# Performance work log

Measured on AMD Instinct MI355X. Metric: run time of the kernel, lower is better.

The kernel has to match this reference:

```python
import jax, jax.numpy as jnp
import numpy as np
from jax import lax

IMG_H, IMG_W = 800, 800
FM_H, FM_W = 50, 50
SIZES = (32.0, 64.0, 128.0)
RATIOS = (0.5, 1.0, 2.0)
A = len(SIZES) * len(RATIOS)          # 9 anchors per location
PRE_NMS = 512
POST_NMS = 128
MIN_SCORE = 0.5
IOU_THRESH = 0.7
MIN_SIZE = 0.001


def gen_anchor_boxes():
    """Anchors in (x1,y1,x2,y2), location-major / anchor-minor ordering
    (matches the permute(0,2,1).reshape(-1,4) layout of the offsets)."""
    sy, sx = IMG_H / FM_H, IMG_W / FM_W
    cy = (np.arange(FM_H) + 0.5) * sy
    cx = (np.arange(FM_W) + 0.5) * sx
    whs = []
    for s in SIZES:
        for r in RATIOS:
            h = s * np.sqrt(r)
            w = s / np.sqrt(r)
            whs.append((w, h))
    whs = np.asarray(whs, np.float32)                      # [A,2]
    cyg, cxg = np.meshgrid(cy, cx, indexing='ij')          # [H,W]
    ctr = np.stack([cxg, cyg], -1)[:, :, None, :]          # [H,W,1,2] (cx,cy)
    half = whs[None, None] / 2.0                           # [1,1,A,2]
    boxes = np.concatenate([ctr - half, ctr + half], -1)   # [H,W,A,4]
    return jnp.asarray(boxes.reshape(-1, 4), jnp.float32)  # [H*W*A,4]


def conv2d(x, w, b, pad):
    y = lax.conv_general_dilated(x, w, (1, 1), [(pad, pad), (pad, pad)],
                                 dimension_numbers=('NCHW', 'OIHW', 'NCHW'))
    return y + b[None, :, None, None]


def decode_boxes(offsets, anchors):
    """offsets [B,N,4] = (dx,dy,dw,dh); anchors [N,4] corners -> corners."""
    aw = anchors[:, 2] - anchors[:, 0]
    ah = anchors[:, 3] - anchors[:, 1]
    acx = anchors[:, 0] + 0.5 * aw
    acy = anchors[:, 1] + 0.5 * ah
    px = acx + offsets[..., 0] * aw
    py = acy + offsets[..., 1] * ah
    pw = aw * jnp.exp(offsets[..., 2])
    ph = ah * jnp.exp(offsets[..., 3])
    return jnp.stack([px - 0.5 * pw, py - 0.5 * ph,
                      px + 0.5 * pw, py + 0.5 * ph], -1)


def proposals_one_image(boxes, scores):
    """boxes [N,4], scores [N] -> padded ([POST_NMS,4],[POST_NMS])."""
    s, idx = lax.top_k(scores, PRE_NMS)          # pre-NMS top-k (sorted desc)
    b = boxes[idx]                               # [PRE,4]
    b = jnp.stack([jnp.clip(b[:, 0], 0.0, IMG_W),
                   jnp.clip(b[:, 1], 0.0, IMG_H),
                   jnp.clip(b[:, 2], 0.0, IMG_W),
                   jnp.clip(b[:, 3], 0.0, IMG_H)], -1)
    w = b[:, 2] - b[:, 0]
    h = b[:, 3] - b[:, 1]
    valid = (w >= MIN_SIZE) & (h >= MIN_SIZE) & (s >= MIN_SCORE)
    # pairwise IoU (NMS decisions are discrete -> stop_gradient)
    bi = lax.stop_gradient(b)
    area = (bi[:, 2] - bi[:, 0]) * (bi[:, 3] - bi[:, 1])
    lt = jnp.maximum(bi[:, None, :2], bi[None, :, :2])
    rb = jnp.minimum(bi[:, None, 2:], bi[None, :, 2:])
    wh = jnp.clip(rb - lt, 0.0)
    inter = wh[..., 0] * wh[..., 1]
    iou = inter / (area[:, None] + area[None, :] - inter + 1e-9)
    rng = jnp.arange(PRE_NMS)

    def body(keep, i):
        sup = (iou[i] > IOU_THRESH) & (rng > i) & keep[i]
        return keep & ~sup, None

    keep, _ = lax.scan(body, valid, rng)         # greedy NMS over sorted cands
    masked = jnp.where(keep, s, -1.0)
    top_s, top_i = lax.top_k(masked, POST_NMS)   # kept boxes keep score order
    ok = top_s >= MIN_SCORE
    out_b = b[top_i] * ok[:, None].astype(b.dtype)
    out_s = jnp.where(ok, top_s, 0.0)
    return out_b, out_s


def rpn_forward(feature_maps, w1, b1, w2, b2, w3, b3):
    B = feature_maps.shape[0]
    shared = jax.nn.relu(conv2d(feature_maps, w1, b1, 1))      # [B,512,H,W]
    cls = jax.nn.sigmoid(conv2d(shared, w2, b2, 0))            # [B,A,H,W]
    off = conv2d(shared, w3, b3, 0)                            # [B,4A,H,W]
    # location-major, anchor-minor flattening (matches torch permute/reshape)
    scores = cls.reshape(B, A, -1).transpose(0, 2, 1).reshape(B, -1)        # [B,N]
    offsets = off.reshape(B, 4 * A, -1).transpose(0, 2, 1).reshape(B, -1, 4)
    anchors = gen_anchor_boxes()
    boxes = decode_boxes(offsets, anchors)                     # [B,N,4]
    return jax.vmap(proposals_one_image)(boxes, scores)        # padded outputs


def setup_inputs() -> dict:
    key = jax.random.key(0)
    ks = jax.random.split(key, 4)
    fm = jax.random.normal(ks[0], (16, 512, FM_H, FM_W), jnp.float32)
    w1 = jax.random.normal(ks[1], (512, 512, 3, 3), jnp.float32) * 0.02
    b1 = jnp.zeros((512,), jnp.float32)
    w2 = jax.random.normal(ks[2], (9, 512, 1, 1), jnp.float32) * 0.05
    b2 = jnp.zeros((9,), jnp.float32)
    w3 = jax.random.normal(ks[3], (36, 512, 1, 1), jnp.float32) * 0.01
    b3 = jnp.zeros((36,), jnp.float32)
    return {"feature_maps": fm, "w1": w1, "b1": b1, "w2": w2, "b2": b2,
            "w3": w3, "b3": b3}


def reference(feature_maps, w1, b1, w2, b2, w3, b3):
    return rpn_forward(feature_maps, w1, b1, w2, b2, w3, b3)
```

## Files before the change

### kernel.cpp

```cpp
#include <hip/hip_runtime.h>
#include <math.h>
#include <stdint.h>

#define FMW 50
#define P_IMG 2500
#define CIN 512
#define NANCH 22500
#define BATCH 16
#define PRE 512
#define POST 128
#define NCHUNK 44
#define NPAD (NCHUNK * 512)
#define MB 192
#define NTIL 14
#define WIN 320

typedef __attribute__((ext_vector_type(8))) short short8;
typedef __attribute__((ext_vector_type(16))) float f32x16;

union U4S8 { uint4 u; short8 s; };

__device__ __forceinline__ unsigned short f2bf(float x) {
    unsigned u = __float_as_uint(x);
    unsigned r = u + 0x7FFFu + ((u >> 16) & 1u);
    return (unsigned short)(r >> 16);
}
__device__ __forceinline__ float bf2f(unsigned short h) {
    return __uint_as_float(((unsigned)h) << 16);
}

__device__ __forceinline__ void gload_lds16(const void* g, void* l) {
    __builtin_amdgcn_global_load_lds(
        (const __attribute__((address_space(1))) void*)g,
        (__attribute__((address_space(3))) void*)l, 16, 0, 0);
}

__global__ void k_prepack(const float* __restrict__ w1, char* __restrict__ w1pack) {
    int t = blockIdx.x * 256 + threadIdx.x;
    int l = t & 63;
    int NT = (t >> 6) & 15;
    int c = (t >> 10) & 31;
    int pos = t >> 15;
    int oc = NT * 32 + (l & 31);
    unsigned short hv[8], lv[8];
#pragma unroll
    for (int j = 0; j < 8; ++j) {
        int ci = c * 16 + (l >> 5) * 8 + j;
        float x = w1[((size_t)oc * 512 + ci) * 9 + pos];
        unsigned short h = f2bf(x);
        hv[j] = h;
        lv[j] = f2bf(x - bf2f(h));
    }
    size_t base = ((size_t)((pos * 32 + c) * 16 + NT) * 2) * 1024 + (size_t)l * 16;
    uint4 hu, lu;
    hu.x = hv[0] | ((unsigned)hv[1] << 16); hu.y = hv[2] | ((unsigned)hv[3] << 16);
    hu.z = hv[4] | ((unsigned)hv[5] << 16); hu.w = hv[6] | ((unsigned)hv[7] << 16);
    lu.x = lv[0] | ((unsigned)lv[1] << 16); lu.y = lv[2] | ((unsigned)lv[3] << 16);
    lu.z = lv[4] | ((unsigned)lv[5] << 16); lu.w = lv[6] | ((unsigned)lv[7] << 16);
    *(uint4*)(w1pack + base) = hu;
    *(uint4*)(w1pack + base + 1024) = lu;
}

__global__ __launch_bounds__(512, 2)
void k_conv_mfma(const float* __restrict__ fm, const char* __restrict__ w1pack,
                 const float* __restrict__ b1, const float* __restrict__ w2,
                 const float* __restrict__ b2, const float* __restrict__ w3,
                 const float* __restrict__ b3,
                 float* __restrict__ off_ws, unsigned long long* __restrict__ keys) {
    __shared__ __align__(16) char smem[123392];

    const int t = threadIdx.x;
    const int l = t & 63;
    const int w = t >> 6;
    const int r = w >> 2;
    const int q = w & 3;
    const int img = blockIdx.x / NTIL;
    const int p0 = (blockIdx.x % NTIL) * MB;

    f32x16 acc[3][4];
#pragma unroll
    for (int mt = 0; mt < 3; ++mt)
#pragma unroll
        for (int nt = 0; nt < 4; ++nt)
#pragma unroll
            for (int g = 0; g < 16; ++g) acc[mt][nt][g] = 0.f;

    int xs[3];
#pragma unroll
    for (int mt = 0; mt < 3; ++mt) xs[mt] = (p0 + r * 96 + mt * 32 + (l & 31)) % FMW;

    const int arb = (64 + r * 96 + (l & 31)) * 32 + (l >> 5) * 16;
    const size_t img_base = (size_t)img * CIN * P_IMG;
    const int DPOS[9] = {-51, -50, -49, -1, 0, 1, 49, 50, 51};

    char* Abuf = smem;
    char* Bb0 = smem + 20480;
    char* Bb1 = smem + 53248;

    auto stageA = [&](int cc) {
#pragma unroll
        for (int i = 0; i < 3; ++i) {
            int flat = i * 512 + t;
            if (flat < 1280) {
                int qq = flat & 3;
                int pxl = flat >> 2;
                int pw = p0 - 64 + pxl;
                bool ok = (pw >= 0) && (pw < P_IMG);
                float v[4];
#pragma unroll
                for (int k = 0; k < 4; ++k)
                    v[k] = ok ? fm[img_base + (size_t)(cc * 16 + qq * 4 + k) * P_IMG + pw] : 0.f;
                unsigned short h[4], lo[4];
#pragma unroll
                for (int k = 0; k < 4; ++k) {
                    h[k] = f2bf(v[k]);
                    lo[k] = f2bf(v[k] - bf2f(h[k]));
                }
                uint2 hu, lu;
                hu.x = h[0] | ((unsigned)h[1] << 16);  hu.y = h[2] | ((unsigned)h[3] << 16);
                lu.x = lo[0] | ((unsigned)lo[1] << 16); lu.y = lo[2] | ((unsigned)lo[3] << 16);
                *(uint2*)(Abuf + pxl * 32 + qq * 8) = hu;
                *(uint2*)(Abuf + 10240 + pxl * 32 + qq * 8) = lu;
            }
        }
    };

    auto stageB = [&](int kk) {
        int c = kk / 9, pos = kk % 9;
        const char* src = w1pack + (size_t)(pos * 32 + c) * 32768;
        char* dst = (kk & 1) ? Bb1 : Bb0;
#pragma unroll
        for (int j = 0; j < 4; ++j) {
            int chunk = w * 4 + j;
            gload_lds16(src + chunk * 1024 + l * 16, dst + chunk * 1024);
        }
    };

    stageB(0);
    stageA(0);
    __syncthreads();

    for (int kk = 0; kk < 288; ++kk) {
        const int c = kk / 9, pos = kk % 9;
        if (kk + 1 < 288) stageB(kk + 1);

        const int dpos = DPOS[pos];
        const int dx = pos % 3 - 1;
        U4S8 ah[3], al[3];
        const char* ap = Abuf + arb + dpos * 32;
#pragma unroll
        for (int mt = 0; mt < 3; ++mt) {
            ah[mt].u = *(const uint4*)(ap + mt * 1024);
            al[mt].u = *(const uint4*)(ap + 10240 + mt * 1024);
            bool xok = (dx == 0) || (dx < 0 ? (xs[mt] > 0) : (xs[mt] < FMW - 1));
            if (!xok) {
                ah[mt].u.x = 0; ah[mt].u.y = 0; ah[mt].u.z = 0; ah[mt].u.w = 0;
                al[mt].u.x = 0; al[mt].u.y = 0; al[mt].u.z = 0; al[mt].u.w = 0;
            }
        }
        const char* bp = ((kk & 1) ? Bb1 : Bb0) + q * 8192 + l * 16;
#pragma unroll
        for (int nt = 0; nt < 4; ++nt) {
            U4S8 bh, bl;
            bh.u = *(const uint4*)(bp + nt * 2048);
            bl.u = *(const uint4*)(bp + nt * 2048 + 1024);
#pragma unroll
            for (int mt = 0; mt < 3; ++mt) {
                acc[mt][nt] = __builtin_amdgcn_mfma_f32_32x32x16_bf16(ah[mt].s, bh.s, acc[mt][nt], 0, 0, 0);
                acc[mt][nt] = __builtin_amdgcn_mfma_f32_32x32x16_bf16(al[mt].s, bh.s, acc[mt][nt], 0, 0, 0);
                acc[mt][nt] = __builtin_amdgcn_mfma_f32_32x32x16_bf16(ah[mt].s, bl.s, acc[mt][nt], 0, 0, 0);
            }
        }

        if (pos == 8 && c < 31) {
            __syncthreads();
            stageA(c + 1);
        }
        __syncthreads();
    }

    float* SH = (float*)smem;
    float* W  = (float*)(smem + 98816);
    float b1v[4];
#pragma unroll
    for (int nt = 0; nt < 4; ++nt) b1v[nt] = b1[q * 128 + nt * 32 + (l & 31)];

    const int pxe = t % 192;
    const int og = t / 192;
    const int no = (og == 0) ? 23 : 22;
    float p45[23];
#pragma unroll
    for (int m = 0; m < 23; ++m) p45[m] = 0.f;

    for (int rr = 0; rr < 4; ++rr) {
        __syncthreads();
#pragma unroll
        for (int i = 0; i < 12; ++i) {
            int e = i * 512 + t;
            if (e < 5760) {
                int o = e >> 7, cl = e & 127;
                W[o * 128 + cl] = (o < 9) ? w2[o * 512 + rr * 128 + cl]
                                          : w3[(o - 9) * 512 + rr * 128 + cl];
            }
        }
        if (q == rr) {
#pragma unroll
            for (int nt = 0; nt < 4; ++nt) {
                int oc_l = nt * 32 + (l & 31);
#pragma unroll
                for (int mt = 0; mt < 3; ++mt)
#pragma unroll
                    for (int g = 0; g < 16; ++g) {
                        int row = (g & 3) + 8 * (g >> 2) + 4 * (l >> 5);
                        SH[oc_l * 193 + r * 96 + mt * 32 + row] =
                            fmaxf(acc[mt][nt][g] + b1v[nt], 0.f);
                    }
            }
        }
        __syncthreads();
        if (og < 2) {
            for (int cl = 0; cl < 128; ++cl) {
                float sv = SH[cl * 193 + pxe];
#pragma unroll
                for (int m = 0; m < 23; ++m)
                    if (m < no) p45[m] = fmaf(sv, W[(og * 23 + m) * 128 + cl], p45[m]);
            }
        }
    }

    const int pE = p0 + pxe;
    if (og < 2 && pE < P_IMG) {
        for (int m = 0; m < no; ++m) {
            int o = og * 23 + m;
            if (o < 9) {
                float z = p45[m] + b2[o];
                float s = (z >= 0.f) ? (1.f / (1.f + expf(-z)))
                                     : (expf(z) / (1.f + expf(z)));
                unsigned n = (unsigned)(pE * 9 + o);
                unsigned long long key =
                    ((unsigned long long)__float_as_uint(s) << 32) |
                    (unsigned long long)(0xFFFFFFFFu - n);
                keys[(size_t)img * NPAD + n] = key;
            } else {
                int cc = o - 9;
                off_ws[((size_t)img * P_IMG + pE) * 36 + cc] = p45[m] + b3[cc];
            }
        }
    }
}

__global__ __launch_bounds__(256)
void k_sort_chunks(unsigned long long* __restrict__ keys) {
    __shared__ unsigned long long sk[512];
    const int t = threadIdx.x;
    const int img = blockIdx.x / NCHUNK;
    const int ch = blockIdx.x % NCHUNK;
    const size_t base = (size_t)img * NPAD + ch * 512;
    int a0 = ch * 512 + t, a1 = ch * 512 + t + 256;
    sk[t] = (a0 < NANCH) ? keys[base + t] : 0ull;
    sk[t + 256] = (a1 < NANCH) ? keys[base + t + 256] : 0ull;
    for (int k = 2; k <= 512; k <<= 1)
        for (int j = k >> 1; j > 0; j >>= 1) {
            __syncthreads();
            for (int i = t; i < 512; i += 256) {
                int lx = i ^ j;
                if (lx > i) {
                    unsigned long long a = sk[i], b = sk[lx];
                    bool desc = ((i & k) == 0);
                    if (desc ? (a < b) : (a > b)) { sk[i] = b; sk[lx] = a; }
                }
            }
        }
    __syncthreads();
    keys[base + t] = sk[t];
    keys[base + t + 256] = sk[t + 256];
}

__global__ __launch_bounds__(256)
void k_nms(const unsigned long long* __restrict__ keys,
           const float* __restrict__ off_ws, float* __restrict__ out) {
    __shared__ unsigned long long top[512];
    __shared__ unsigned long long chk[512];
    __shared__ float bx1[512], by1[512], bx2[512], by2[512], bar[512], bsc[512];
    __shared__ int keep[512];

    const int t = threadIdx.x;
    const int img = blockIdx.x;
    const size_t kbase = (size_t)img * NPAD;

    top[t] = keys[kbase + t];
    top[t + 256] = keys[kbase + t + 256];

    for (int c = 1; c < NCHUNK; ++c) {
        __syncthreads();
        chk[t] = keys[kbase + c * 512 + t];
        chk[t + 256] = keys[kbase + c * 512 + t + 256];
        __syncthreads();
        for (int i = t; i < 512; i += 256) {
            unsigned long long a = top[i], b = chk[511 - i];
            top[i] = (a > b) ? a : b;
        }
        for (int j = 256; j > 0; j >>= 1) {
            __syncthreads();
            int i = ((t & ~(j - 1)) << 1) | (t & (j - 1));
            unsigned long long a = top[i], b = top[i + j];
            if (a < b) { top[i] = b; top[i + j] = a; }
        }
    }
    __syncthreads();

    for (int i = t; i < 512; i += 256) {
        unsigned long long key = top[i];
        float s = __uint_as_float((unsigned)(key >> 32));
        unsigned id = 0xFFFFFFFFu - (unsigned)(key & 0xFFFFFFFFull);
        float x1 = 0.f, y1 = 0.f, x2 = 0.f, y2 = 0.f;
        bool valid = false;
        if (key != 0ull && id < (unsigned)NANCH) {
            int p = id / 9, a = id - p * 9;
            int gy = p / FMW, gx = p - gy * FMW;
            const double SS[3] = {32.0, 64.0, 128.0};
            const double RR[3] = {0.5, 1.0, 2.0};
            double sq = sqrt(RR[a % 3]);
            float wa32 = (float)(SS[a / 3] / sq);
            float ha32 = (float)(SS[a / 3] * sq);
            double cx = ((double)gx + 0.5) * 16.0;
            double cy = ((double)gy + 0.5) * 16.0;
            float ax1 = (float)(cx - (double)(wa32 * 0.5f));
            float ay1 = (float)(cy - (double)(ha32 * 0.5f));
            float ax2 = (float)(cx + (double)(wa32 * 0.5f));
            float ay2 = (float)(cy + (double)(ha32 * 0.5f));
            float aw = ax2 - ax1, ah2 = ay2 - ay1;
            float acx = ax1 + 0.5f * aw, acy = ay1 + 0.5f * ah2;
            const float4 off = *(const float4*)(off_ws + ((size_t)img * P_IMG + p) * 36 + a * 4);
            float px = acx + off.x * aw;
            float py = acy + off.y * ah2;
            float pw = aw * expf(off.z);
            float ph = ah2 * expf(off.w);
            x1 = fminf(fmaxf(px - 0.5f * pw, 0.f), 800.f);
            y1 = fminf(fmaxf(py - 0.5f * ph, 0.f), 800.f);
            x2 = fminf(fmaxf(px + 0.5f * pw, 0.f), 800.f);
            y2 = fminf(fmaxf(py + 0.5f * ph, 0.f), 800.f);
            float ww = x2 - x1, hh = y2 - y1;
            valid = (ww >= 1e-3f) && (hh >= 1e-3f) && (s >= 0.5f);
        }
        bx1[i] = x1; by1[i] = y1; bx2[i] = x2; by2[i] = y2;
        bar[i] = (x2 - x1) * (y2 - y1);
        bsc[i] = s;
        keep[i] = valid ? 1 : 0;
    }
    __syncthreads();

    for (int i = 0; i < PRE - 1; ++i) {
        __syncthreads();
        if (keep[i] == 0) continue;
        float xi1 = bx1[i], yi1 = by1[i], xi2 = bx2[i], yi2 = by2[i], ai = bar[i];
        for (int j = i + 1 + t; j < PRE; j += 256) {
            if (keep[j]) {
                float lx = fmaxf(xi1, bx1[j]);
                float ly = fmaxf(yi1, by1[j]);
                float rx = fminf(xi2, bx2[j]);
                float ry = fminf(yi2, by2[j]);
                float iw = fmaxf(rx - lx, 0.f);
                float ih = fmaxf(ry - ly, 0.f);
                float inter = iw * ih;
                float iou = inter / (ai + bar[j] - inter + 1e-9f);
                if (iou > 0.7f) keep[j] = 0;
            }
        }
    }
    __syncthreads();

    for (int i = t; i < 512; i += 256) {
        float m = keep[i] ? bsc[i] : -1.0f;
        unsigned u = __float_as_uint(m);
        u = (u & 0x80000000u) ? ~u : (u | 0x80000000u);
        chk[i] = ((unsigned long long)u << 32) | (unsigned long long)(511 - i);
    }
    for (int k = 2; k <= 512; k <<= 1)
        for (int j = k >> 1; j > 0; j >>= 1) {
            __syncthreads();
            for (int i = t; i < 512; i += 256) {
                int lx = i ^ j;
                if (lx > i) {
                    unsigned long long a = chk[i], b = chk[lx];
                    bool desc = ((i & k) == 0);
                    if (desc ? (a < b) : (a > b)) { chk[i] = b; chk[lx] = a; }
                }
            }
        }
    __syncthreads();

    if (t < POST) {
        unsigned long long key = chk[t];
        int slot = 511 - (int)(key & 0xFFFFFFFFull);
        float m = keep[slot] ? bsc[slot] : -1.0f;
        bool ok = (m >= 0.5f);
        float* ob = out + ((size_t)img * POST + t) * 4;
        ob[0] = ok ? bx1[slot] : 0.f;
        ob[1] = ok ? by1[slot] : 0.f;
        ob[2] = ok ? bx2[slot] : 0.f;
        ob[3] = ok ? by2[slot] : 0.f;
        out[(size_t)BATCH * POST * 4 + img * POST + t] = ok ? m : 0.f;
    }
}

extern "C" void kernel_launch(void* const* d_in, const int* in_sizes, int n_in,
                              void* d_out, int out_size, void* d_ws, size_t ws_size,
                              hipStream_t stream) {
    const float* fm = (const float*)d_in[0];
    const float* w1 = (const float*)d_in[1];
    const float* b1 = (const float*)d_in[2];
    const float* w2 = (const float*)d_in[3];
    const float* b2 = (const float*)d_in[4];
    const float* w3 = (const float*)d_in[5];
    const float* b3 = (const float*)d_in[6];
    float* out = (float*)d_out;

    char* ws = (char*)d_ws;
    char* w1pack = ws;
    float* off_ws = (float*)(ws + 0x900000);
    unsigned long long* keys = (unsigned long long*)(ws + 0xE80000);

    k_prepack<<<1152, 256, 0, stream>>>(w1, w1pack);
    k_conv_mfma<<<BATCH * NTIL, 512, 0, stream>>>(fm, w1pack, b1, w2, b2, w3, b3, off_ws, keys);
    k_sort_chunks<<<BATCH * NCHUNK, 256, 0, stream>>>(keys);
    k_nms<<<BATCH, 256, 0, stream>>>(keys, off_ws, out);
}
```

Before: 1.129 ms.

## Halve conv pixel tile to 96 and re-split waves across output channels

Shrinks the per-block pixel tile from 192 to 96, so the grid grows from 14 to 27 tiles per image. Each of the 8 waves now owns 64 output channels over all 96 pixels, instead of 128 channels over 96 pixels. LDS per block and accumulators per thread are cut so that 4 blocks can be resident per CU, and MFMA issue is wrapped in s_setprio. The 1x1 head epilogue is redistributed as 5 groups of 9 outputs. The tradeoff is more halo re-staging of A per pixel and B weight tiles reloaded by twice as many blocks.

Result: slower. 1.210 ms (+7.2%).

```diff
diff --git a/kernel.cpp b/kernel.cpp
--- a/kernel.cpp
+++ b/kernel.cpp
@@ -11,9 +11,12 @@
 #define POST 128
 #define NCHUNK 44
 #define NPAD (NCHUNK * 512)
-#define MB 192
-#define NTIL 14
-#define WIN 320
+#define MB 96
+#define NTIL 27
+#define WIN 224
+#define ASP 7168
+#define ABYTES 14336
+#define BOFF 14336
 
 typedef __attribute__((ext_vector_type(8))) short short8;
 typedef __attribute__((ext_vector_type(16))) float f32x16;
@@ -61,47 +64,43 @@
     *(uint4*)(w1pack + base + 1024) = lu;
 }
 
-__global__ __launch_bounds__(512, 2)
+__global__ __launch_bounds__(512, 4)
 void k_conv_mfma(const float* __restrict__ fm, const char* __restrict__ w1pack,
                  const float* __restrict__ b1, const float* __restrict__ w2,
                  const float* __restrict__ b2, const float* __restrict__ w3,
                  const float* __restrict__ b3,
                  float* __restrict__ off_ws, unsigned long long* __restrict__ keys) {
-    __shared__ __align__(16) char smem[123392];
+    __shared__ __align__(16) char smem[79872];
 
     const int t = threadIdx.x;
     const int l = t & 63;
     const int w = t >> 6;
-    const int r = w >> 2;
-    const int q = w & 3;
     const int img = blockIdx.x / NTIL;
     const int p0 = (blockIdx.x % NTIL) * MB;
 
-    f32x16 acc[3][4];
+    f32x16 acc[3][2];
 #pragma unroll
     for (int mt = 0; mt < 3; ++mt)
 #pragma unroll
-        for (int nt = 0; nt < 4; ++nt)
+        for (int nt = 0; nt < 2; ++nt)
 #pragma unroll
             for (int g = 0; g < 16; ++g) acc[mt][nt][g] = 0.f;
 
     int xs[3];
 #pragma unroll
-    for (int mt = 0; mt < 3; ++mt) xs[mt] = (p0 + r * 96 + mt * 32 + (l & 31)) % FMW;
-
-    const int arb = (64 + r * 96 + (l & 31)) * 32 + (l >> 5) * 16;
+    for (int mt = 0; mt < 3; ++mt) xs[mt] = (p0 + mt * 32 + (l & 31)) % FMW;
+
+    const int arb = (64 + (l & 31)) * 32 + (l >> 5) * 16;
     const size_t img_base = (size_t)img * CIN * P_IMG;
     const int DPOS[9] = {-51, -50, -49, -1, 0, 1, 49, 50, 51};
 
     char* Abuf = smem;
-    char* Bb0 = smem + 20480;
-    char* Bb1 = smem + 53248;
 
     auto stageA = [&](int cc) {
 #pragma unroll
-        for (int i = 0; i < 3; ++i) {
+        for (int i = 0; i < 2; ++i) {
             int flat = i * 512 + t;
-            if (flat < 1280) {
+            if (flat < 896) {
                 int qq = flat & 3;
                 int pxl = flat >> 2;
                 int pw = p0 - 64 + pxl;
@@ -120,7 +119,7 @@
                 hu.x = h[0] | ((unsigned)h[1] << 16);  hu.y = h[2] | ((unsigned)h[3] << 16);
                 lu.x = lo[0] | ((unsigned)lo[1] << 16); lu.y = lo[2] | ((unsigned)lo[3] << 16);
                 *(uint2*)(Abuf + pxl * 32 + qq * 8) = hu;
-                *(uint2*)(Abuf + 10240 + pxl * 32 + qq * 8) = lu;
+                *(uint2*)(Abuf + ASP + pxl * 32 + qq * 8) = lu;
             }
         }
     };
@@ -128,7 +127,7 @@
     auto stageB = [&](int kk) {
         int c = kk / 9, pos = kk % 9;
         const char* src = w1pack + (size_t)(pos * 32 + c) * 32768;
-        char* dst = (kk & 1) ? Bb1 : Bb0;
+        char* dst = smem + BOFF + (kk & 1) * 32768;
 #pragma unroll
         for (int j = 0; j < 4; ++j) {
             int chunk = w * 4 + j;
@@ -151,16 +150,17 @@
 #pragma unroll
         for (int mt = 0; mt < 3; ++mt) {
             ah[mt].u = *(const uint4*)(ap + mt * 1024);
-            al[mt].u = *(const uint4*)(ap + 10240 + mt * 1024);
+            al[mt].u = *(const uint4*)(ap + ASP + mt * 1024);
             bool xok = (dx == 0) || (dx < 0 ? (xs[mt] > 0) : (xs[mt] < FMW - 1));
             if (!xok) {
                 ah[mt].u.x = 0; ah[mt].u.y = 0; ah[mt].u.z = 0; ah[mt].u.w = 0;
                 al[mt].u.x = 0; al[mt].u.y = 0; al[mt].u.z = 0; al[mt].u.w = 0;
             }
         }
-        const char* bp = ((kk & 1) ? Bb1 : Bb0) + q * 8192 + l * 16;
-#pragma unroll
-        for (int nt = 0; nt < 4; ++nt) {
+        const char* bp = smem + BOFF + (kk & 1) * 32768 + w * 4096 + l * 16;
+        __builtin_amdgcn_s_setprio(1);
+#pragma unroll
+        for (int nt = 0; nt < 2; ++nt) {
             U4S8 bh, bl;
             bh.u = *(const uint4*)(bp + nt * 2048);
             bl.u = *(const uint4*)(bp + nt * 2048 + 1024);
@@ -171,6 +171,7 @@
                 acc[mt][nt] = __builtin_amdgcn_mfma_f32_32x32x16_bf16(ah[mt].s, bl.s, acc[mt][nt], 0, 0, 0);
             }
         }
+        __builtin_amdgcn_s_setprio(0);
 
         if (pos == 8 && c < 31) {
             __syncthreads();
@@ -180,17 +181,16 @@
     }
 
     float* SH = (float*)smem;
-    float* W  = (float*)(smem + 98816);
-    float b1v[4];
-#pragma unroll
-    for (int nt = 0; nt < 4; ++nt) b1v[nt] = b1[q * 128 + nt * 32 + (l & 31)];
-
-    const int pxe = t % 192;
-    const int og = t / 192;
-    const int no = (og == 0) ? 23 : 22;
-    float p45[23];
-#pragma unroll
-    for (int m = 0; m < 23; ++m) p45[m] = 0.f;
+    float* W  = (float*)(smem + 49664);
+    float b1v[2];
+#pragma unroll
+    for (int nt = 0; nt < 2; ++nt) b1v[nt] = b1[w * 64 + nt * 32 + (l & 31)];
+
+    const int pxe = t % 96;
+    const int og = t / 96;
+    float p45[9];
+#pragma unroll
+    for (int m = 0; m < 9; ++m) p45[m] = 0.f;
 
     for (int rr = 0; rr < 4; ++rr) {
         __syncthreads();
@@ -203,35 +203,36 @@
                                           : w3[(o - 9) * 512 + rr * 128 + cl];
             }
         }
-        if (q == rr) {
-#pragma unroll
-            for (int nt = 0; nt < 4; ++nt) {
-                int oc_l = nt * 32 + (l & 31);
+        if ((w >> 1) == rr) {
+#pragma unroll
+            for (int nt = 0; nt < 2; ++nt) {
+                int oc_l = (w & 1) * 64 + nt * 32 + (l & 31);
 #pragma unroll
                 for (int mt = 0; mt < 3; ++mt)
 #pragma unroll
                     for (int g = 0; g < 16; ++g) {
                         int row = (g & 3) + 8 * (g >> 2) + 4 * (l >> 5);
-                        SH[oc_l * 193 + r * 96 + mt * 32 + row] =
+                        SH[oc_l * 97 + mt * 32 + row] =
                             fmaxf(acc[mt][nt][g] + b1v[nt], 0.f);
                     }
             }
         }
         __syncthreads();
-        if (og < 2) {
+        if (og < 5) {
             for (int cl = 0; cl < 128; ++cl) {
-                float sv = SH[cl * 193 + pxe];
-#pragma unroll
-                for (int m = 0; m < 23; ++m)
-                    if (m < no) p45[m] = fmaf(sv, W[(og * 23 + m) * 128 + cl], p45[m]);
+                float sv = SH[cl * 97 + pxe];
+#pragma unroll
+                for (int m = 0; m < 9; ++m)
+                    p45[m] = fmaf(sv, W[(og * 9 + m) * 128 + cl], p45[m]);
             }
         }
     }
 
     const int pE = p0 + pxe;
-    if (og < 2 && pE < P_IMG) {
-        for (int m = 0; m < no; ++m) {
-            int o = og * 23 + m;
+    if (og < 5 && pE < P_IMG) {
+#pragma unroll
+        for (int m = 0; m < 9; ++m) {
+            int o = og * 9 + m;
             if (o < 9) {
                 float z = p45[m] + b2[o];
                 float s = (z >= 0.f) ? (1.f / (1.f + expf(-z)))
```

## Load conv weight fragments straight to registers with double-buffered prefetch

Applied to the files above, without the earlier changes.

The B (weight) operand is no longer staged through LDS with global_load_lds and a per-iteration block barrier. Each wave now loads its own weight fragments directly from global memory into registers, double-buffered across two unrolled iterations. Block barriers remain only where the A tile is restaged, and s_setprio is raised around the MFMA bursts. This removes most of the barriers and LDS traffic, at the cost of more VGPR pressure, which could cause spills at launch_bounds(512,2), and of exposed global load latency.

Result: slower. 2.011 ms (+78.2%).

```diff
diff --git a/kernel.cpp b/kernel.cpp
--- a/kernel.cpp
+++ b/kernel.cpp
@@ -29,12 +29,6 @@
     return __uint_as_float(((unsigned)h) << 16);
 }
 
-__device__ __forceinline__ void gload_lds16(const void* g, void* l) {
-    __builtin_amdgcn_global_load_lds(
-        (const __attribute__((address_space(1))) void*)g,
-        (__attribute__((address_space(3))) void*)l, 16, 0, 0);
-}
-
 __global__ void k_prepack(const float* __restrict__ w1, char* __restrict__ w1pack) {
     int t = blockIdx.x * 256 + threadIdx.x;
     int l = t & 63;
@@ -61,6 +55,63 @@
     *(uint4*)(w1pack + base + 1024) = lu;
 }
 
+#define LOADB(kk, H0, H1, H2, H3, L0, L1, L2, L3)                               \
+    {                                                                           \
+        const char* src_ = wq + (size_t)((((kk) % 9) * 32 + (kk) / 9)) * 32768; \
+        H0 = *(const uint4*)(src_);        L0 = *(const uint4*)(src_ + 1024);   \
+        H1 = *(const uint4*)(src_ + 2048); L1 = *(const uint4*)(src_ + 3072);   \
+        H2 = *(const uint4*)(src_ + 4096); L2 = *(const uint4*)(src_ + 5120);   \
+        H3 = *(const uint4*)(src_ + 6144); L3 = *(const uint4*)(src_ + 7168);   \
+    }
+
+#define MFMA3(NT, BH, BL)                                                                     \
+    {                                                                                         \
+        U4S8 bh_, bl_;                                                                        \
+        bh_.u = BH; bl_.u = BL;                                                               \
+        _Pragma("unroll")                                                                     \
+        for (int mt = 0; mt < 3; ++mt) {                                                      \
+            acc[mt][NT] = __builtin_amdgcn_mfma_f32_32x32x16_bf16(ah_[mt].s, bh_.s, acc[mt][NT], 0, 0, 0); \
+            acc[mt][NT] = __builtin_amdgcn_mfma_f32_32x32x16_bf16(al_[mt].s, bh_.s, acc[mt][NT], 0, 0, 0); \
+            acc[mt][NT] = __builtin_amdgcn_mfma_f32_32x32x16_bf16(ah_[mt].s, bl_.s, acc[mt][NT], 0, 0, 0); \
+        }                                                                                     \
+    }
+
+#define COMPUTE(kk, H0, H1, H2, H3, L0, L1, L2, L3)                       \
+    {                                                                     \
+        const int pos_ = (kk) % 9;                                        \
+        const int dx_ = pos_ % 3 - 1;                                     \
+        const int dposv_ = (pos_ / 3 - 1) * FMW + dx_;                    \
+        U4S8 ah_[3], al_[3];                                              \
+        const char* ap_ = Abuf + arb + dposv_ * 32;                       \
+        _Pragma("unroll")                                                 \
+        for (int mt = 0; mt < 3; ++mt) {                                  \
+            ah_[mt].u = *(const uint4*)(ap_ + mt * 1024);                 \
+            al_[mt].u = *(const uint4*)(ap_ + 10240 + mt * 1024);         \
+            bool xok = (dx_ == 0) || (dx_ < 0 ? (xs[mt] > 0) : (xs[mt] < FMW - 1)); \
+            if (!xok) {                                                   \
+                ah_[mt].u.x = 0; ah_[mt].u.y = 0; ah_[mt].u.z = 0; ah_[mt].u.w = 0; \
+                al_[mt].u.x = 0; al_[mt].u.y = 0; al_[mt].u.z = 0; al_[mt].u.w = 0; \
+            }                                                             \
+        }                                                                 \
+        __builtin_amdgcn_s_setprio(1);                                    \
+        MFMA3(0, H0, L0); MFMA3(1, H1, L1); MFMA3(2, H2, L2); MFMA3(3, H3, L3); \
+        __builtin_amdgcn_s_setprio(0);                                    \
+    }
+
+#define MAYBE_STAGEA(kk)                                                  \
+    {                                                                     \
+        const int posA_ = (kk) % 9, cA_ = (kk) / 9;                       \
+        if (posA_ == 8 && cA_ < 31) {                                     \
+            asm volatile("" ::: "memory");                                \
+            __builtin_amdgcn_s_barrier();                                 \
+            asm volatile("" ::: "memory");                                \
+            stageA(cA_ + 1);                                              \
+            asm volatile("s_waitcnt lgkmcnt(0)" ::: "memory");            \
+            __builtin_amdgcn_s_barrier();                                 \
+            asm volatile("" ::: "memory");                                \
+        }                                                                 \
+    }
+
 __global__ __launch_bounds__(512, 2)
 void k_conv_mfma(const float* __restrict__ fm, const char* __restrict__ w1pack,
                  const float* __restrict__ b1, const float* __restrict__ w2,
@@ -91,11 +142,8 @@
 
     const int arb = (64 + r * 96 + (l & 31)) * 32 + (l >> 5) * 16;
     const size_t img_base = (size_t)img * CIN * P_IMG;
-    const int DPOS[9] = {-51, -50, -49, -1, 0, 1, 49, 50, 51};
 
     char* Abuf = smem;
-    char* Bb0 = smem + 20480;
-    char* Bb1 = smem + 53248;
 
     auto stageA = [&](int cc) {
 #pragma unroll
@@ -125,58 +173,23 @@
         }
     };
 
-    auto stageB = [&](int kk) {
-        int c = kk / 9, pos = kk % 9;
-        const char* src = w1pack + (size_t)(pos * 32 + c) * 32768;
-        char* dst = (kk & 1) ? Bb1 : Bb0;
-#pragma unroll
-        for (int j = 0; j < 4; ++j) {
-            int chunk = w * 4 + j;
-            gload_lds16(src + chunk * 1024 + l * 16, dst + chunk * 1024);
-        }
-    };
-
-    stageB(0);
+    const char* wq = w1pack + q * 8192 + (size_t)l * 16;
+
+    uint4 pH0, pH1, pH2, pH3, pL0, pL1, pL2, pL3;
+    uint4 oH0, oH1, oH2, oH3, oL0, oL1, oL2, oL3;
+
     stageA(0);
-    __syncthreads();
-
-    for (int kk = 0; kk < 288; ++kk) {
-        const int c = kk / 9, pos = kk % 9;
-        if (kk + 1 < 288) stageB(kk + 1);
-
-        const int dpos = DPOS[pos];
-        const int dx = pos % 3 - 1;
-        U4S8 ah[3], al[3];
-        const char* ap = Abuf + arb + dpos * 32;
-#pragma unroll
-        for (int mt = 0; mt < 3; ++mt) {
-            ah[mt].u = *(const uint4*)(ap + mt * 1024);
-            al[mt].u = *(const uint4*)(ap + 10240 + mt * 1024);
-            bool xok = (dx == 0) || (dx < 0 ? (xs[mt] > 0) : (xs[mt] < FMW - 1));
-            if (!xok) {
-                ah[mt].u.x = 0; ah[mt].u.y = 0; ah[mt].u.z = 0; ah[mt].u.w = 0;
-                al[mt].u.x = 0; al[mt].u.y = 0; al[mt].u.z = 0; al[mt].u.w = 0;
-            }
-        }
-        const char* bp = ((kk & 1) ? Bb1 : Bb0) + q * 8192 + l * 16;
-#pragma unroll
-        for (int nt = 0; nt < 4; ++nt) {
-            U4S8 bh, bl;
-            bh.u = *(const uint4*)(bp + nt * 2048);
-            bl.u = *(const uint4*)(bp + nt * 2048 + 1024);
-#pragma unroll
-            for (int mt = 0; mt < 3; ++mt) {
-                acc[mt][nt] = __builtin_amdgcn_mfma_f32_32x32x16_bf16(ah[mt].s, bh.s, acc[mt][nt], 0, 0, 0);
-                acc[mt][nt] = __builtin_amdgcn_mfma_f32_32x32x16_bf16(al[mt].s, bh.s, acc[mt][nt], 0, 0, 0);
-                acc[mt][nt] = __builtin_amdgcn_mfma_f32_32x32x16_bf16(ah[mt].s, bl.s, acc[mt][nt], 0, 0, 0);
-            }
-        }
-
-        if (pos == 8 && c < 31) {
-            __syncthreads();
-            stageA(c + 1);
-        }
-        __syncthreads();
+    LOADB(0, pH0, pH1, pH2, pH3, pL0, pL1, pL2, pL3);
+    __syncthreads();
+
+    for (int kp = 0; kp < 144; ++kp) {
+        const int kk0 = 2 * kp;
+        LOADB(kk0 + 1, oH0, oH1, oH2, oH3, oL0, oL1, oL2, oL3);
+        COMPUTE(kk0, pH0, pH1, pH2, pH3, pL0, pL1, pL2, pL3);
+        MAYBE_STAGEA(kk0);
+        if (kp < 143) LOADB(kk0 + 2, pH0, pH1, pH2, pH3, pL0, pL1, pL2, pL3);
+        COMPUTE(kk0 + 1, oH0, oH1, oH2, oH3, oL0, oL1, oL2, oL3);
+        MAYBE_STAGEA(kk0 + 1);
     }
 
     float* SH = (float*)smem;
```

## Replace serial NMS loop with parallel IoU bitmask and single-wave sweep

Applied to the files above, without the earlier changes.

Rewrites the NMS from a 511-iteration loop with a block-wide barrier per step into two phases. First, each thread computes a 512-bit suppression mask for its boxes against all others. Then a single wavefront sweeps the masks serially, using shuffles to read keep bits. This removes hundreds of __syncthreads, but computes the full 512x512 IoU matrix (no early skip of suppressed boxes) and adds about 36KB of shared memory, which may lower occupancy.

After: 1.067 ms. 1.06x faster.

```diff
diff --git a/kernel.cpp b/kernel.cpp
--- a/kernel.cpp
+++ b/kernel.cpp
@@ -283,6 +283,8 @@
     __shared__ unsigned long long chk[512];
     __shared__ float bx1[512], by1[512], bx2[512], by2[512], bar[512], bsc[512];
     __shared__ int keep[512];
+    __shared__ unsigned long long sup[512][9];
+    __shared__ unsigned long long kmask[8];
 
     const int t = threadIdx.x;
     const int img = blockIdx.x;
@@ -350,12 +352,13 @@
     }
     __syncthreads();
 
-    for (int i = 0; i < PRE - 1; ++i) {
-        __syncthreads();
-        if (keep[i] == 0) continue;
+    for (int i = t; i < 512; i += 256) {
         float xi1 = bx1[i], yi1 = by1[i], xi2 = bx2[i], yi2 = by2[i], ai = bar[i];
-        for (int j = i + 1 + t; j < PRE; j += 256) {
-            if (keep[j]) {
+#pragma unroll
+        for (int wd = 0; wd < 8; ++wd) {
+            unsigned long long bits = 0ull;
+            for (int b = 0; b < 64; ++b) {
+                int j = wd * 64 + b;
                 float lx = fmaxf(xi1, bx1[j]);
                 float ly = fmaxf(yi1, by1[j]);
                 float rx = fminf(xi2, bx2[j]);
@@ -364,10 +367,33 @@
                 float ih = fmaxf(ry - ly, 0.f);
                 float inter = iw * ih;
                 float iou = inter / (ai + bar[j] - inter + 1e-9f);
-                if (iou > 0.7f) keep[j] = 0;
-            }
-        }
-    }
+                if ((iou > 0.7f) && (j > i)) bits |= (1ull << b);
+            }
+            sup[i][wd] = bits;
+        }
+    }
+    if (t < 8) {
+        unsigned long long m = 0ull;
+#pragma unroll
+        for (int b = 0; b < 64; ++b)
+            if (keep[t * 64 + b]) m |= (1ull << b);
+        kmask[t] = m;
+    }
+    __syncthreads();
+
+    if (t < 64) {
+        unsigned long long m = (t < 8) ? kmask[t] : 0ull;
+        for (int i = 0; i < 512; ++i) {
+            unsigned long long mw = __shfl(m, i >> 6);
+            if ((mw >> (i & 63)) & 1ull) {
+                if (t < 8) m &= ~sup[i][t];
+            }
+        }
+        if (t < 8) kmask[t] = m;
+    }
+    __syncthreads();
+    for (int i = t; i < 512; i += 256)
+        keep[i] = (int)((kmask[i >> 6] >> (i & 63)) & 1ull);
     __syncthreads();
 
     for (int i = t; i < 512; i += 256) {
```
